# Optimization experiments

Hardware: AMD Instinct MI355X
Metric: run time of the kernel (lower is better)

The kernel has to match this reference:

```python
import jax, jax.numpy as jnp
import numpy as np

B, T, C, E = 4, 2048, 1024, 8  # batch, seq, n_embd, num_experts


def setup_inputs() -> dict:
    key = jax.random.key(0)
    k_x, k_wr, k_we = jax.random.split(key, 3)
    x = jax.random.normal(k_x, (B, T, C), dtype=jnp.float32)
    # router: Linear(C, E); scale chosen so softmax gates spread around the 0.5 threshold
    Wr = jax.random.normal(k_wr, (E, C), dtype=jnp.float32) * 0.05
    br = jnp.zeros((E,), dtype=jnp.float32)
    # experts: E x Linear(C, C), y = x @ W^T + b
    We = jax.random.normal(k_we, (E, C, C), dtype=jnp.float32) * (1.0 / np.sqrt(C))
    be = jnp.zeros((E, C), dtype=jnp.float32)
    return {"x": x, "Wr": Wr, "br": br, "We": We, "be": be}


def reference(x, Wr, br, We, be):
    # router logits + softmax gates: [B, T, E]
    logits = jnp.einsum('btc,ec->bte', x, Wr) + br
    gates = jax.nn.softmax(logits, axis=-1)
    # hard selection: token goes through expert e iff gate_e > 0.5 (at most one
    # expert per token since gates sum to 1); output is NOT scaled by the gate.
    mask = (gates > 0.5).astype(x.dtype)  # [B, T, E]
    # all-expert outputs (torch Linear: y = x @ W^T + b): [B, T, E, C]
    h = jnp.einsum('btc,edc->bted', x, We) + be
    # masked combine -> [B, T, C]; unrouted tokens stay zero like torch.zeros_like
    return jnp.einsum('bted,bte->btd', h, mask)
```

## Files before the change

kernel.cpp:

```cpp
#include <hip/hip_runtime.h>
#include <hip/hip_bf16.h>
#include <stdint.h>

#define NB 4
#define NT 2048
#define NC 1024
#define NE 8
#define NTOK (NB * NT)
#define MAXT (NTOK / 128 + NE - 1)
#define CSTRIDE 32

typedef __attribute__((ext_vector_type(4))) float floatx4;
typedef __attribute__((ext_vector_type(8))) __bf16 bf16x8;
typedef unsigned short ushort_t;

#define AS1 __attribute__((address_space(1)))
#define AS3 __attribute__((address_space(3)))

__device__ __forceinline__ ushort_t f2bf(float f) {
    uint32_t u = __builtin_bit_cast(uint32_t, f);
    u += 0x7FFFu + ((u >> 16) & 1u);
    return (ushort_t)(u >> 16);
}

__global__ void zero_counts_k(int* __restrict__ counts) {
    if (threadIdx.x < NE) counts[threadIdx.x * CSTRIDE] = 0;
}

__global__ __launch_bounds__(256, 6) void router_k(
    const float* __restrict__ x, const float* __restrict__ Wr,
    const float* __restrict__ br, float* __restrict__ out,
    int* __restrict__ counts, int* __restrict__ buckets,
    ushort_t* __restrict__ xbf ,
    const float* __restrict__ We, ushort_t* __restrict__ webf )
{
    const int wave = threadIdx.x >> 6;
    const int lane = threadIdx.x & 63;
    const int tok  = blockIdx.x * 4 + wave;

    const size_t cbase = ((size_t)(blockIdx.x * 256 + threadIdx.x)) * 8;
    float4 cva0, cvb0, cva1, cvb1;
    if (webf) {
        cva0 = *(const float4*)(We + cbase);
        cvb0 = *(const float4*)(We + cbase + 4);
        cva1 = *(const float4*)(We + cbase + 4194304);
        cvb1 = *(const float4*)(We + cbase + 4194304 + 4);
    }

    const float4* xr = (const float4*)(x + (size_t)tok * NC);
    float4 xv[4];
#pragma unroll
    for (int j = 0; j < 4; ++j) xv[j] = xr[lane + 64 * j];

    float acc[NE];
#pragma unroll
    for (int e = 0; e < NE; ++e) {
        const float4* wr = (const float4*)(Wr + e * NC);
        float a = 0.f;
#pragma unroll
        for (int j = 0; j < 4; ++j) {
            float4 w = wr[lane + 64 * j];
            a += xv[j].x * w.x; a += xv[j].y * w.y;
            a += xv[j].z * w.z; a += xv[j].w * w.w;
        }
        acc[e] = a;
    }
#pragma unroll
    for (int off = 32; off >= 1; off >>= 1)
#pragma unroll
        for (int e = 0; e < NE; ++e) acc[e] += __shfl_xor(acc[e], off);

#pragma unroll
    for (int e = 0; e < NE; ++e) acc[e] += br[e];

    float lmax = acc[0]; int emax = 0;
#pragma unroll
    for (int e = 1; e < NE; ++e) if (acc[e] > lmax) { lmax = acc[e]; emax = e; }
    float S = 0.f;
#pragma unroll
    for (int e = 0; e < NE; ++e) S += expf(acc[e] - lmax);

    const bool routed = (S < 2.0f);
    if (routed) {
        if (xbf) {
            typedef __attribute__((ext_vector_type(4))) __bf16 bf16x4;
            union { bf16x4 v; ushort_t s[4]; } p;
#pragma unroll
            for (int j = 0; j < 4; ++j) {
                p.s[0] = f2bf(xv[j].x); p.s[1] = f2bf(xv[j].y);
                p.s[2] = f2bf(xv[j].z); p.s[3] = f2bf(xv[j].w);
                *(bf16x4*)(xbf + (size_t)tok * NC + (lane + 64 * j) * 4) = p.v;
            }
        }
        if (lane == 0) {
            int pos = atomicAdd(&counts[emax * CSTRIDE], 1);
            buckets[emax * NTOK + pos] = tok;
        }
    } else {
        float4 z = make_float4(0.f, 0.f, 0.f, 0.f);
        float4* orow = (float4*)(out + (size_t)tok * NC);
#pragma unroll
        for (int j = 0; j < 4; ++j) orow[lane + 64 * j] = z;
    }

    if (webf) {
        union { bf16x8 v; ushort_t s[8]; } p;
        p.s[0] = f2bf(cva0.x); p.s[1] = f2bf(cva0.y); p.s[2] = f2bf(cva0.z); p.s[3] = f2bf(cva0.w);
        p.s[4] = f2bf(cvb0.x); p.s[5] = f2bf(cvb0.y); p.s[6] = f2bf(cvb0.z); p.s[7] = f2bf(cvb0.w);
        *(bf16x8*)(webf + cbase) = p.v;
        p.s[0] = f2bf(cva1.x); p.s[1] = f2bf(cva1.y); p.s[2] = f2bf(cva1.z); p.s[3] = f2bf(cva1.w);
        p.s[4] = f2bf(cvb1.x); p.s[5] = f2bf(cvb1.y); p.s[6] = f2bf(cvb1.z); p.s[7] = f2bf(cvb1.w);
        *(bf16x8*)(webf + cbase + 4194304) = p.v;
    }
}

__device__ __forceinline__ void gload_lds16(const void* g, void* l) {
    __builtin_amdgcn_global_load_lds((const AS1 unsigned int*)g,
                                     (AS3 unsigned int*)l, 16, 0, 0);
}

__global__ __launch_bounds__(256) void moe_gemm_bf16_k(
    const ushort_t* __restrict__ xbf, const ushort_t* __restrict__ webf,
    const float* __restrict__ be, float* __restrict__ out,
    const int* __restrict__ counts, const int* __restrict__ buckets)
{
    int cw[NE];
#pragma unroll
    for (int i = 0; i < NE; ++i) cw[i] = counts[i * CSTRIDE];
    const int t = blockIdx.x;
    int base = 0, e = -1, m0 = 0;
#pragma unroll
    for (int i = 0; i < NE; ++i) {
        const int te = (cw[i] + 127) >> 7;
        if (e < 0 && t < base + te) { e = i; m0 = (t - base) << 7; }
        base += te;
    }
    if (e < 0) return;
    const int cnt = cw[e];
    const int n0  = blockIdx.y * 128;

    __shared__ ushort_t As[128 * 64];
    __shared__ ushort_t Bs[128 * 64];

    const int tid   = threadIdx.x;
    const int wave  = tid >> 6, lane = tid & 63;
    const int chunk = tid & 7;
    const int rbase = tid >> 3;

    const ushort_t* asrc[4];
    const ushort_t* bsrc[4];
#pragma unroll
    for (int i = 0; i < 4; ++i) {
        const int row = i * 32 + rbase;
        const int sc  = chunk ^ (row & 7);
        int mi = m0 + row; if (mi >= cnt) mi = cnt - 1;
        const int tok = buckets[e * NTOK + mi];
        asrc[i] = xbf + (size_t)tok * NC + sc * 8;
        bsrc[i] = webf + ((size_t)(e * 1024 + n0 + row)) * NC + sc * 8;
    }

    const int wm = (wave >> 1) * 64, wn = (wave & 1) * 64;
    const int fr = lane & 15, hi = lane >> 4;

    floatx4 acc[4][4];
#pragma unroll
    for (int m = 0; m < 4; ++m)
#pragma unroll
        for (int n = 0; n < 4; ++n) acc[m][n] = (floatx4)(0.0f);

    for (int k0 = 0; k0 < NC; k0 += 64) {
#pragma unroll
        for (int i = 0; i < 4; ++i)
            gload_lds16(asrc[i] + k0, &As[(i * 256 + tid) * 8]);
#pragma unroll
        for (int i = 0; i < 4; ++i)
            gload_lds16(bsrc[i] + k0, &Bs[(i * 256 + tid) * 8]);
        __syncthreads();
#pragma unroll
        for (int ks = 0; ks < 2; ++ks) {
            bf16x8 af[4], bfv[4];
#pragma unroll
            for (int m = 0; m < 4; ++m) {
                const int row = wm + m * 16 + fr;
                const int cg  = (ks * 4 + hi) ^ (row & 7);
                af[m] = *(const bf16x8*)((const char*)As + row * 128 + cg * 16);
            }
#pragma unroll
            for (int n = 0; n < 4; ++n) {
                const int row = wn + n * 16 + fr;
                const int cg  = (ks * 4 + hi) ^ (row & 7);
                bfv[n] = *(const bf16x8*)((const char*)Bs + row * 128 + cg * 16);
            }
#pragma unroll
            for (int m = 0; m < 4; ++m)
#pragma unroll
                for (int n = 0; n < 4; ++n)
                    acc[m][n] = __builtin_amdgcn_mfma_f32_16x16x32_bf16(
                        af[m], bfv[n], acc[m][n], 0, 0, 0);
        }
        __syncthreads();
    }

    const int r4 = (lane >> 4) * 4;
    float bev[4];
#pragma unroll
    for (int n = 0; n < 4; ++n) bev[n] = be[e * NC + n0 + wn + n * 16 + fr];
#pragma unroll
    for (int m = 0; m < 4; ++m) {
#pragma unroll
        for (int j = 0; j < 4; ++j) {
            const int trow = m0 + wm + m * 16 + r4 + j;
            if (trow < cnt) {
                const int tok = buckets[e * NTOK + trow];
                float* orow = out + (size_t)tok * NC + n0 + wn + fr;
#pragma unroll
                for (int n = 0; n < 4; ++n) orow[n * 16] = acc[m][n][j] + bev[n];
            }
        }
    }
}

#define BM 64
#define BN 64
#define BK 32
#define LPAD 40
__global__ __launch_bounds__(256) void moe_gemm_k(
    const float* __restrict__ x, const float* __restrict__ We,
    const float* __restrict__ be, float* __restrict__ out,
    const int* __restrict__ counts, const int* __restrict__ buckets)
{
    const int e   = blockIdx.z;
    const int cnt = counts[e * CSTRIDE];
    const int m0  = blockIdx.x * BM;
    if (m0 >= cnt) return;
    const int n0  = blockIdx.y * BN;

    __shared__ ushort_t As[BM * LPAD];
    __shared__ ushort_t Bs[BM * LPAD];

    const int tid  = threadIdx.x;
    const int srow = tid >> 2;
    const int scg  = (tid & 3) * 8;

    const int mrow = m0 + srow;
    const int tokA = (mrow < cnt) ? buckets[e * NTOK + mrow] : -1;
    const float* xrow = x + (size_t)(tokA < 0 ? 0 : tokA) * NC;
    const float* wrow = We + ((size_t)e * NC + (n0 + srow)) * NC;

    const int wave = tid >> 6, lane = tid & 63;
    const int wm = (wave >> 1) * 32, wn = (wave & 1) * 32;
    const int fr = lane & 15;
    const int fk = (lane >> 4) * 8;

    floatx4 acc[2][2];
#pragma unroll
    for (int m = 0; m < 2; ++m)
#pragma unroll
        for (int n = 0; n < 2; ++n) acc[m][n] = (floatx4)(0.0f);

    for (int k0 = 0; k0 < NC; k0 += BK) {
        float4 a0 = make_float4(0.f,0.f,0.f,0.f), a1 = a0;
        if (tokA >= 0) {
            a0 = *(const float4*)(xrow + k0 + scg);
            a1 = *(const float4*)(xrow + k0 + scg + 4);
        }
        float4 b0 = *(const float4*)(wrow + k0 + scg);
        float4 b1 = *(const float4*)(wrow + k0 + scg + 4);

        __syncthreads();
        union { bf16x8 v; ushort_t s[8]; } pa, pb;
        pa.s[0] = f2bf(a0.x); pa.s[1] = f2bf(a0.y); pa.s[2] = f2bf(a0.z); pa.s[3] = f2bf(a0.w);
        pa.s[4] = f2bf(a1.x); pa.s[5] = f2bf(a1.y); pa.s[6] = f2bf(a1.z); pa.s[7] = f2bf(a1.w);
        pb.s[0] = f2bf(b0.x); pb.s[1] = f2bf(b0.y); pb.s[2] = f2bf(b0.z); pb.s[3] = f2bf(b0.w);
        pb.s[4] = f2bf(b1.x); pb.s[5] = f2bf(b1.y); pb.s[6] = f2bf(b1.z); pb.s[7] = f2bf(b1.w);
        *(bf16x8*)&As[srow * LPAD + scg] = pa.v;
        *(bf16x8*)&Bs[srow * LPAD + scg] = pb.v;
        __syncthreads();

        bf16x8 af[2], bfr[2];
#pragma unroll
        for (int m = 0; m < 2; ++m)
            af[m] = *(const bf16x8*)&As[(wm + m * 16 + fr) * LPAD + fk];
#pragma unroll
        for (int n = 0; n < 2; ++n)
            bfr[n] = *(const bf16x8*)&Bs[(wn + n * 16 + fr) * LPAD + fk];
#pragma unroll
        for (int m = 0; m < 2; ++m)
#pragma unroll
            for (int n = 0; n < 2; ++n)
                acc[m][n] = __builtin_amdgcn_mfma_f32_16x16x32_bf16(af[m], bfr[n], acc[m][n], 0, 0, 0);
    }

    const int r4 = (lane >> 4) * 4;
#pragma unroll
    for (int m = 0; m < 2; ++m) {
        const int trowb = m0 + wm + m * 16 + r4;
#pragma unroll
        for (int j = 0; j < 4; ++j) {
            const int trow = trowb + j;
            if (trow < cnt) {
                const int tok = buckets[e * NTOK + trow];
#pragma unroll
                for (int n = 0; n < 2; ++n) {
                    const int d = n0 + wn + n * 16 + fr;
                    out[(size_t)tok * NC + d] = acc[m][n][j] + be[e * NC + d];
                }
            }
        }
    }
}

extern "C" void kernel_launch(void* const* d_in, const int* in_sizes, int n_in,
                              void* d_out, int out_size, void* d_ws, size_t ws_size,
                              hipStream_t stream)
{
    const float* x  = (const float*)d_in[0];
    const float* Wr = (const float*)d_in[1];
    const float* br = (const float*)d_in[2];
    const float* We = (const float*)d_in[3];
    const float* be = (const float*)d_in[4];
    float* out = (float*)d_out;

    int* counts  = (int*)d_ws;
    int* buckets = (int*)((char*)d_ws + 1024);
    const size_t XBF_OFF = 263168;
    const size_t WBF_OFF = 17040384;
    const size_t WS_NEED = 33817600;
    const bool fast = (ws_size >= WS_NEED);

    ushort_t* xbf  = fast ? (ushort_t*)((char*)d_ws + XBF_OFF) : nullptr;
    ushort_t* webf = fast ? (ushort_t*)((char*)d_ws + WBF_OFF) : nullptr;

    hipLaunchKernelGGL(zero_counts_k, dim3(1), dim3(64), 0, stream, counts);
    hipLaunchKernelGGL(router_k, dim3(NTOK / 4), dim3(256), 0, stream,
                       x, Wr, br, out, counts, buckets, xbf, We, webf);
    if (fast) {
        hipLaunchKernelGGL(moe_gemm_bf16_k, dim3(MAXT, NC / 128, 1), dim3(256),
                           0, stream, xbf, webf, be, out, counts, buckets);
    } else {
        hipLaunchKernelGGL(moe_gemm_k, dim3(NTOK / BM, NC / BN, NE), dim3(256),
                           0, stream, x, We, be, out, counts, buckets);
    }
}
```

Before: 66.28 us.

## Fuse bf16 conversion into expert GEMM and batch router over four tokens per wave

Drops the separate pass in the router that converted all of We and the routed x rows to bf16 in workspace. The expert GEMM now loads fp32 x and We directly, converts them to bf16 in registers and writes them into the swizzled LDS tiles, replacing the async global-to-LDS loads and dropping the now-redundant trailing barrier. The router processes four tokens per wave, so each Wr load is reused across four tokens, and the small-workspace fallback GEMM is removed. The aim is to avoid the full-weight write and read-back round trip, at the cost of GEMM tiles reading twice the bytes, repeating the conversion in every N block, and exposing load latency without async copies.

```diff
diff --git a/kernel.cpp b/kernel.cpp
--- a/kernel.cpp
+++ b/kernel.cpp
@@ -9,13 +9,11 @@
 #define NTOK (NB * NT)
 #define MAXT (NTOK / 128 + NE - 1)
 #define CSTRIDE 32
+#define RBLK 512
 
 typedef __attribute__((ext_vector_type(4))) float floatx4;
 typedef __attribute__((ext_vector_type(8))) __bf16 bf16x8;
 typedef unsigned short ushort_t;
-
-#define AS1 __attribute__((address_space(1)))
-#define AS3 __attribute__((address_space(3)))
 
 __device__ __forceinline__ ushort_t f2bf(float f) {
     uint32_t u = __builtin_bit_cast(uint32_t, f);
@@ -27,100 +25,84 @@
     if (threadIdx.x < NE) counts[threadIdx.x * CSTRIDE] = 0;
 }
 
-__global__ __launch_bounds__(256, 6) void router_k(
+__global__ __launch_bounds__(256, 4) void router_zero_k(
     const float* __restrict__ x, const float* __restrict__ Wr,
     const float* __restrict__ br, float* __restrict__ out,
-    int* __restrict__ counts, int* __restrict__ buckets,
-    ushort_t* __restrict__ xbf ,
-    const float* __restrict__ We, ushort_t* __restrict__ webf )
+    int* __restrict__ counts, int* __restrict__ buckets)
 {
     const int wave = threadIdx.x >> 6;
     const int lane = threadIdx.x & 63;
-    const int tok  = blockIdx.x * 4 + wave;
-
-    const size_t cbase = ((size_t)(blockIdx.x * 256 + threadIdx.x)) * 8;
-    float4 cva0, cvb0, cva1, cvb1;
-    if (webf) {
-        cva0 = *(const float4*)(We + cbase);
-        cvb0 = *(const float4*)(We + cbase + 4);
-        cva1 = *(const float4*)(We + cbase + 4194304);
-        cvb1 = *(const float4*)(We + cbase + 4194304 + 4);
-    }
-
-    const float4* xr = (const float4*)(x + (size_t)tok * NC);
-    float4 xv[4];
-#pragma unroll
-    for (int j = 0; j < 4; ++j) xv[j] = xr[lane + 64 * j];
-
-    float acc[NE];
-#pragma unroll
-    for (int e = 0; e < NE; ++e) {
-        const float4* wr = (const float4*)(Wr + e * NC);
-        float a = 0.f;
-#pragma unroll
-        for (int j = 0; j < 4; ++j) {
-            float4 w = wr[lane + 64 * j];
-            a += xv[j].x * w.x; a += xv[j].y * w.y;
-            a += xv[j].z * w.z; a += xv[j].w * w.w;
-        }
-        acc[e] = a;
-    }
+    const int tb   = (blockIdx.x * 4 + wave) * 4;
+
+    float acc[4][NE];
+#pragma unroll
+    for (int t = 0; t < 4; ++t)
+#pragma unroll
+        for (int e = 0; e < NE; ++e) acc[t][e] = 0.f;
+
+#pragma unroll
+    for (int h = 0; h < 2; ++h) {
+        float4 xv[4][2];
+#pragma unroll
+        for (int t = 0; t < 4; ++t) {
+            const float4* xr = (const float4*)(x + (size_t)(tb + t) * NC);
+#pragma unroll
+            for (int jh = 0; jh < 2; ++jh)
+                xv[t][jh] = xr[lane + 64 * (h * 2 + jh)];
+        }
+#pragma unroll
+        for (int e = 0; e < NE; ++e) {
+            const float4* wr = (const float4*)(Wr + e * NC);
+            float4 w0 = wr[lane + 64 * (h * 2 + 0)];
+            float4 w1 = wr[lane + 64 * (h * 2 + 1)];
+#pragma unroll
+            for (int t = 0; t < 4; ++t) {
+                float a = acc[t][e];
+                a += xv[t][0].x * w0.x; a += xv[t][0].y * w0.y;
+                a += xv[t][0].z * w0.z; a += xv[t][0].w * w0.w;
+                a += xv[t][1].x * w1.x; a += xv[t][1].y * w1.y;
+                a += xv[t][1].z * w1.z; a += xv[t][1].w * w1.w;
+                acc[t][e] = a;
+            }
+        }
+    }
+
 #pragma unroll
     for (int off = 32; off >= 1; off >>= 1)
 #pragma unroll
-        for (int e = 0; e < NE; ++e) acc[e] += __shfl_xor(acc[e], off);
-
-#pragma unroll
-    for (int e = 0; e < NE; ++e) acc[e] += br[e];
-
-    float lmax = acc[0]; int emax = 0;
-#pragma unroll
-    for (int e = 1; e < NE; ++e) if (acc[e] > lmax) { lmax = acc[e]; emax = e; }
-    float S = 0.f;
-#pragma unroll
-    for (int e = 0; e < NE; ++e) S += expf(acc[e] - lmax);
-
-    const bool routed = (S < 2.0f);
-    if (routed) {
-        if (xbf) {
-            typedef __attribute__((ext_vector_type(4))) __bf16 bf16x4;
-            union { bf16x4 v; ushort_t s[4]; } p;
-#pragma unroll
-            for (int j = 0; j < 4; ++j) {
-                p.s[0] = f2bf(xv[j].x); p.s[1] = f2bf(xv[j].y);
-                p.s[2] = f2bf(xv[j].z); p.s[3] = f2bf(xv[j].w);
-                *(bf16x4*)(xbf + (size_t)tok * NC + (lane + 64 * j) * 4) = p.v;
-            }
-        }
-        if (lane == 0) {
-            int pos = atomicAdd(&counts[emax * CSTRIDE], 1);
-            buckets[emax * NTOK + pos] = tok;
-        }
-    } else {
-        float4 z = make_float4(0.f, 0.f, 0.f, 0.f);
-        float4* orow = (float4*)(out + (size_t)tok * NC);
-#pragma unroll
-        for (int j = 0; j < 4; ++j) orow[lane + 64 * j] = z;
-    }
-
-    if (webf) {
-        union { bf16x8 v; ushort_t s[8]; } p;
-        p.s[0] = f2bf(cva0.x); p.s[1] = f2bf(cva0.y); p.s[2] = f2bf(cva0.z); p.s[3] = f2bf(cva0.w);
-        p.s[4] = f2bf(cvb0.x); p.s[5] = f2bf(cvb0.y); p.s[6] = f2bf(cvb0.z); p.s[7] = f2bf(cvb0.w);
-        *(bf16x8*)(webf + cbase) = p.v;
-        p.s[0] = f2bf(cva1.x); p.s[1] = f2bf(cva1.y); p.s[2] = f2bf(cva1.z); p.s[3] = f2bf(cva1.w);
-        p.s[4] = f2bf(cvb1.x); p.s[5] = f2bf(cvb1.y); p.s[6] = f2bf(cvb1.z); p.s[7] = f2bf(cvb1.w);
-        *(bf16x8*)(webf + cbase + 4194304) = p.v;
-    }
-}
-
-__device__ __forceinline__ void gload_lds16(const void* g, void* l) {
-    __builtin_amdgcn_global_load_lds((const AS1 unsigned int*)g,
-                                     (AS3 unsigned int*)l, 16, 0, 0);
-}
-
-__global__ __launch_bounds__(256) void moe_gemm_bf16_k(
-    const ushort_t* __restrict__ xbf, const ushort_t* __restrict__ webf,
+        for (int t = 0; t < 4; ++t)
+#pragma unroll
+            for (int e = 0; e < NE; ++e) acc[t][e] += __shfl_xor(acc[t][e], off);
+
+#pragma unroll
+    for (int t = 0; t < 4; ++t) {
+#pragma unroll
+        for (int e = 0; e < NE; ++e) acc[t][e] += br[e];
+
+        float lmax = acc[t][0]; int emax = 0;
+#pragma unroll
+        for (int e = 1; e < NE; ++e) if (acc[t][e] > lmax) { lmax = acc[t][e]; emax = e; }
+        float S = 0.f;
+#pragma unroll
+        for (int e = 0; e < NE; ++e) S += expf(acc[t][e] - lmax);
+
+        const bool routed = (S < 2.0f);
+        if (routed) {
+            if (lane == 0) {
+                int pos = atomicAdd(&counts[emax * CSTRIDE], 1);
+                buckets[emax * NTOK + pos] = tb + t;
+            }
+        } else {
+            float4 z = make_float4(0.f, 0.f, 0.f, 0.f);
+            float4* orow = (float4*)(out + (size_t)(tb + t) * NC);
+#pragma unroll
+            for (int j = 0; j < 4; ++j) orow[lane + 64 * j] = z;
+        }
+    }
+}
+
+__global__ __launch_bounds__(256) void moe_gemm_f32_k(
+    const float* __restrict__ x, const float* __restrict__ We,
     const float* __restrict__ be, float* __restrict__ out,
     const int* __restrict__ counts, const int* __restrict__ buckets)
 {
@@ -147,16 +129,16 @@
     const int chunk = tid & 7;
     const int rbase = tid >> 3;
 
-    const ushort_t* asrc[4];
-    const ushort_t* bsrc[4];
+    const float* asrc[4];
+    const float* bsrc[4];
 #pragma unroll
     for (int i = 0; i < 4; ++i) {
         const int row = i * 32 + rbase;
         const int sc  = chunk ^ (row & 7);
         int mi = m0 + row; if (mi >= cnt) mi = cnt - 1;
         const int tok = buckets[e * NTOK + mi];
-        asrc[i] = xbf + (size_t)tok * NC + sc * 8;
-        bsrc[i] = webf + ((size_t)(e * 1024 + n0 + row)) * NC + sc * 8;
+        asrc[i] = x + (size_t)tok * NC + sc * 8;
+        bsrc[i] = We + ((size_t)(e * 1024 + n0 + row)) * NC + sc * 8;
     }
 
     const int wm = (wave >> 1) * 64, wn = (wave & 1) * 64;
@@ -169,12 +151,29 @@
         for (int n = 0; n < 4; ++n) acc[m][n] = (floatx4)(0.0f);
 
     for (int k0 = 0; k0 < NC; k0 += 64) {
-#pragma unroll
-        for (int i = 0; i < 4; ++i)
-            gload_lds16(asrc[i] + k0, &As[(i * 256 + tid) * 8]);
-#pragma unroll
-        for (int i = 0; i < 4; ++i)
-            gload_lds16(bsrc[i] + k0, &Bs[(i * 256 + tid) * 8]);
+        float4 av[4][2], bv[4][2];
+#pragma unroll
+        for (int i = 0; i < 4; ++i) {
+            av[i][0] = *(const float4*)(asrc[i] + k0);
+            av[i][1] = *(const float4*)(asrc[i] + k0 + 4);
+            bv[i][0] = *(const float4*)(bsrc[i] + k0);
+            bv[i][1] = *(const float4*)(bsrc[i] + k0 + 4);
+        }
+        __syncthreads();
+#pragma unroll
+        for (int i = 0; i < 4; ++i) {
+            union { bf16x8 v; ushort_t s[8]; } pa, pb;
+            pa.s[0] = f2bf(av[i][0].x); pa.s[1] = f2bf(av[i][0].y);
+            pa.s[2] = f2bf(av[i][0].z); pa.s[3] = f2bf(av[i][0].w);
+            pa.s[4] = f2bf(av[i][1].x); pa.s[5] = f2bf(av[i][1].y);
+            pa.s[6] = f2bf(av[i][1].z); pa.s[7] = f2bf(av[i][1].w);
+            pb.s[0] = f2bf(bv[i][0].x); pb.s[1] = f2bf(bv[i][0].y);
+            pb.s[2] = f2bf(bv[i][0].z); pb.s[3] = f2bf(bv[i][0].w);
+            pb.s[4] = f2bf(bv[i][1].x); pb.s[5] = f2bf(bv[i][1].y);
+            pb.s[6] = f2bf(bv[i][1].z); pb.s[7] = f2bf(bv[i][1].w);
+            *(bf16x8*)&As[(i * 256 + tid) * 8] = pa.v;
+            *(bf16x8*)&Bs[(i * 256 + tid) * 8] = pb.v;
+        }
         __syncthreads();
 #pragma unroll
         for (int ks = 0; ks < 2; ++ks) {
@@ -198,7 +197,6 @@
                     acc[m][n] = __builtin_amdgcn_mfma_f32_16x16x32_bf16(
                         af[m], bfv[n], acc[m][n], 0, 0, 0);
         }
-        __syncthreads();
     }
 
     const int r4 = (lane >> 4) * 4;
@@ -215,96 +213,6 @@
                 float* orow = out + (size_t)tok * NC + n0 + wn + fr;
 #pragma unroll
                 for (int n = 0; n < 4; ++n) orow[n * 16] = acc[m][n][j] + bev[n];
-            }
-        }
-    }
-}
-
-#define BM 64
-#define BN 64
-#define BK 32
-#define LPAD 40
-__global__ __launch_bounds__(256) void moe_gemm_k(
-    const float* __restrict__ x, const float* __restrict__ We,
-    const float* __restrict__ be, float* __restrict__ out,
-    const int* __restrict__ counts, const int* __restrict__ buckets)
-{
-    const int e   = blockIdx.z;
-    const int cnt = counts[e * CSTRIDE];
-    const int m0  = blockIdx.x * BM;
-    if (m0 >= cnt) return;
-    const int n0  = blockIdx.y * BN;
-
-    __shared__ ushort_t As[BM * LPAD];
-    __shared__ ushort_t Bs[BM * LPAD];
-
-    const int tid  = threadIdx.x;
-    const int srow = tid >> 2;
-    const int scg  = (tid & 3) * 8;
-
-    const int mrow = m0 + srow;
-    const int tokA = (mrow < cnt) ? buckets[e * NTOK + mrow] : -1;
-    const float* xrow = x + (size_t)(tokA < 0 ? 0 : tokA) * NC;
-    const float* wrow = We + ((size_t)e * NC + (n0 + srow)) * NC;
-
-    const int wave = tid >> 6, lane = tid & 63;
-    const int wm = (wave >> 1) * 32, wn = (wave & 1) * 32;
-    const int fr = lane & 15;
-    const int fk = (lane >> 4) * 8;
-
-    floatx4 acc[2][2];
-#pragma unroll
-    for (int m = 0; m < 2; ++m)
-#pragma unroll
-        for (int n = 0; n < 2; ++n) acc[m][n] = (floatx4)(0.0f);
-
-    for (int k0 = 0; k0 < NC; k0 += BK) {
-        float4 a0 = make_float4(0.f,0.f,0.f,0.f), a1 = a0;
-        if (tokA >= 0) {
-            a0 = *(const float4*)(xrow + k0 + scg);
-            a1 = *(const float4*)(xrow + k0 + scg + 4);
-        }
-        float4 b0 = *(const float4*)(wrow + k0 + scg);
-        float4 b1 = *(const float4*)(wrow + k0 + scg + 4);
-
-        __syncthreads();
-        union { bf16x8 v; ushort_t s[8]; } pa, pb;
-        pa.s[0] = f2bf(a0.x); pa.s[1] = f2bf(a0.y); pa.s[2] = f2bf(a0.z); pa.s[3] = f2bf(a0.w);
-        pa.s[4] = f2bf(a1.x); pa.s[5] = f2bf(a1.y); pa.s[6] = f2bf(a1.z); pa.s[7] = f2bf(a1.w);
-        pb.s[0] = f2bf(b0.x); pb.s[1] = f2bf(b0.y); pb.s[2] = f2bf(b0.z); pb.s[3] = f2bf(b0.w);
-        pb.s[4] = f2bf(b1.x); pb.s[5] = f2bf(b1.y); pb.s[6] = f2bf(b1.z); pb.s[7] = f2bf(b1.w);
-        *(bf16x8*)&As[srow * LPAD + scg] = pa.v;
-        *(bf16x8*)&Bs[srow * LPAD + scg] = pb.v;
-        __syncthreads();
-
-        bf16x8 af[2], bfr[2];
-#pragma unroll
-        for (int m = 0; m < 2; ++m)
-            af[m] = *(const bf16x8*)&As[(wm + m * 16 + fr) * LPAD + fk];
-#pragma unroll
-        for (int n = 0; n < 2; ++n)
-            bfr[n] = *(const bf16x8*)&Bs[(wn + n * 16 + fr) * LPAD + fk];
-#pragma unroll
-        for (int m = 0; m < 2; ++m)
-#pragma unroll
-            for (int n = 0; n < 2; ++n)
-                acc[m][n] = __builtin_amdgcn_mfma_f32_16x16x32_bf16(af[m], bfr[n], acc[m][n], 0, 0, 0);
-    }
-
-    const int r4 = (lane >> 4) * 4;
-#pragma unroll
-    for (int m = 0; m < 2; ++m) {
-        const int trowb = m0 + wm + m * 16 + r4;
-#pragma unroll
-        for (int j = 0; j < 4; ++j) {
-            const int trow = trowb + j;
-            if (trow < cnt) {
-                const int tok = buckets[e * NTOK + trow];
-#pragma unroll
-                for (int n = 0; n < 2; ++n) {
-                    const int d = n0 + wn + n * 16 + fr;
-                    out[(size_t)tok * NC + d] = acc[m][n][j] + be[e * NC + d];
-                }
             }
         }
     }
@@ -323,22 +231,10 @@
 
     int* counts  = (int*)d_ws;
     int* buckets = (int*)((char*)d_ws + 1024);
-    const size_t XBF_OFF = 263168;
-    const size_t WBF_OFF = 17040384;
-    const size_t WS_NEED = 33817600;
-    const bool fast = (ws_size >= WS_NEED);
-
-    ushort_t* xbf  = fast ? (ushort_t*)((char*)d_ws + XBF_OFF) : nullptr;
-    ushort_t* webf = fast ? (ushort_t*)((char*)d_ws + WBF_OFF) : nullptr;
 
     hipLaunchKernelGGL(zero_counts_k, dim3(1), dim3(64), 0, stream, counts);
-    hipLaunchKernelGGL(router_k, dim3(NTOK / 4), dim3(256), 0, stream,
-                       x, Wr, br, out, counts, buckets, xbf, We, webf);
-    if (fast) {
-        hipLaunchKernelGGL(moe_gemm_bf16_k, dim3(MAXT, NC / 128, 1), dim3(256),
-                           0, stream, xbf, webf, be, out, counts, buckets);
-    } else {
-        hipLaunchKernelGGL(moe_gemm_k, dim3(NTOK / BM, NC / BN, NE), dim3(256),
-                           0, stream, x, We, be, out, counts, buckets);
-    }
-}
+    hipLaunchKernelGGL(router_zero_k, dim3(RBLK), dim3(256), 0, stream,
+                       x, Wr, br, out, counts, buckets);
+    hipLaunchKernelGGL(moe_gemm_f32_k, dim3(MAXT, NC / 128, 1), dim3(256),
+                       0, stream, x, We, be, out, counts, buckets);
+}
```

New measurement: 75.98 us. 14.6% more time.
